# Kernel optimization log

Hardware: AMD Instinct MI355X
Metric: run time of the kernel (lower is better)

The kernel has to match this reference:

```python
import jax, jax.numpy as jnp
import numpy as np

B, T, C = 2, 2048, 1024
H, D = 16, 64
EPS = 1e-05
SCALE = 1.0 / np.sqrt(D)


def _rmsnorm(x, w):
    # normalize over last dim (head_dim)
    return w * (x * jax.lax.rsqrt(jnp.mean(x * x, axis=-1, keepdims=True) + EPS))


def setup_inputs() -> dict:
    key = jax.random.key(0)
    ks = jax.random.split(key, 8)
    x = jax.random.normal(ks[0], (B, T, C), dtype=jnp.float32)
    # causal mask, 1 = attend, 0 = masked
    attention_mask = jnp.tril(jnp.ones((T, T), dtype=jnp.int32))[None, None]
    s = 1.0 / np.sqrt(C)
    Wq = jax.random.normal(ks[1], (C, H * D), dtype=jnp.float32) * s
    Wk = jax.random.normal(ks[2], (C, H * D), dtype=jnp.float32) * s
    Wv = jax.random.normal(ks[3], (C, H * D), dtype=jnp.float32) * s
    Wo = jax.random.normal(ks[4], (H * D, C), dtype=jnp.float32) * s
    q_norm_w = jnp.ones((D,), dtype=jnp.float32)
    k_norm_w = jnp.ones((D,), dtype=jnp.float32)
    gate = jnp.ones((1, H, 1, 1), dtype=jnp.float32)
    return {"x": x, "attention_mask": attention_mask, "Wq": Wq, "Wk": Wk,
            "Wv": Wv, "Wo": Wo, "q_norm_w": q_norm_w, "k_norm_w": k_norm_w,
            "gate": gate}


def reference(x, attention_mask, Wq, Wk, Wv, Wo, q_norm_w, k_norm_w, gate):
    Bx, Tx, Cx = x.shape
    vx = x @ Wv                                   # [B,T,H*D] (kept for value residual)
    q = (x @ Wq).reshape(Bx, Tx, H, D).transpose(0, 2, 1, 3)  # [B,H,T,D]
    k = (x @ Wk).reshape(Bx, Tx, H, D).transpose(0, 2, 1, 3)
    v = vx.reshape(Bx, Tx, H, D).transpose(0, 2, 1, 3)
    q = _rmsnorm(q, q_norm_w)
    k = _rmsnorm(k, k_norm_w)
    att = jnp.einsum('bhqd,bhkd->bhqk', q, k) * SCALE
    att = jnp.where(attention_mask == 0, -jnp.inf, att)
    att = jax.nn.softmax(att, axis=-1)
    att = att * gate                              # per-head gating after softmax
    out = jnp.einsum('bhqk,bhkd->bhqd', att, v)
    out = out.transpose(0, 2, 1, 3).reshape(Bx, Tx, Cx)
    out = out + vx                                # value residual
    out = out @ Wo
    return out
```

## Files before the change

kernel.cpp:

```cpp
#include <hip/hip_runtime.h>

#define T_SEQ 2048
#define CDIM 1024
#define NHEAD 16
#define HDIM 64
#define BATCH 2
#define EPSV 1e-5f
#define SCALE 0.125f
#define LOG2E 1.44269504088896f
#define SMAX 16.0f

typedef __attribute__((ext_vector_type(8))) short bf16x8;
typedef __attribute__((ext_vector_type(4))) float f32x4;

__device__ __forceinline__ float b2f(short s) {
  unsigned u = ((unsigned)(unsigned short)s) << 16;
  return __builtin_bit_cast(float, u);
}
__device__ __forceinline__ short f2b(float f) {
  unsigned u = __builtin_bit_cast(unsigned, f);
  unsigned r = (u + 0x7fffu + ((u >> 16) & 1u)) >> 16;
  return (short)r;
}
__device__ __forceinline__ unsigned cvt_pk_bf16(float a, float b) {
  unsigned r;
  asm("v_cvt_pk_bf16_f32 %0, %1, %2" : "=v"(r) : "v"(a), "v"(b));
  return r;
}

__device__ __forceinline__ void gld16(const void* g, void* l) {
  __builtin_amdgcn_global_load_lds((const __attribute__((address_space(1))) unsigned*)g,
                                   (__attribute__((address_space(3))) unsigned*)l, 16, 0, 0);
}

__device__ __forceinline__ int gswz(int row) { return ((row >> 1) ^ (row >> 3)) & 3; }

__device__ __forceinline__ void stage_sw(short* lds, const char* gbase, int gstride,
                                         int w, int l) {
#pragma unroll
  for (int i = 0; i < 2; ++i) {
    int chunk = w * 2048 + i * 1024 + l * 16;
    int row = chunk >> 7;
    int bir = chunk & 127;
    const char* src = gbase + (size_t)row * gstride + (bir ^ ((row & 7) << 4));
    gld16(src, (char*)lds + chunk);
  }
}
__device__ __forceinline__ void stage_sw8(short* lds, const char* gbase, int gstride,
                                          int w, int l) {
  int chunk = w * 1024 + l * 16;
  int row = chunk >> 7;
  int bir = chunk & 127;
  const char* src = gbase + (size_t)row * gstride + (bir ^ ((row & 7) << 4));
  gld16(src, (char*)lds + chunk);
}

__global__ __launch_bounds__(256) void prep(const float* __restrict__ x,
                                            const float* __restrict__ Wq,
                                            const float* __restrict__ Wk,
                                            const float* __restrict__ Wv,
                                            const float* __restrict__ Wo,
                                            short* __restrict__ xb,
                                            short* __restrict__ WT) {
  __shared__ float tile[64][65];
  const int bid = blockIdx.x;
  if (bid < 2048) {
    size_t i = ((size_t)bid * 256 + threadIdx.x) * 8;
    float4 a = *(const float4*)&x[i];
    float4 b = *(const float4*)&x[i + 4];
    short4 lo, hi;
    lo.x = f2b(a.x); lo.y = f2b(a.y); lo.z = f2b(a.z); lo.w = f2b(a.w);
    hi.x = f2b(b.x); hi.y = f2b(b.y); hi.z = f2b(b.z); hi.w = f2b(b.w);
    *(short4*)&xb[i] = lo;
    *(short4*)&xb[i + 4] = hi;
    return;
  }
  const int t = bid - 2048;
  const int z = t >> 8, rem = t & 255;
  const float* W = (z == 0) ? Wq : (z == 1) ? Wk : (z == 2) ? Wv : Wo;
  const int r0 = (rem >> 4) * 64, c0 = (rem & 15) * 64;
  const int tr = threadIdx.x >> 4, tc4 = (threadIdx.x & 15) * 4;
#pragma unroll
  for (int i = 0; i < 4; ++i) {
    float4 v = *(const float4*)&W[(size_t)(r0 + tr + i * 16) * 1024 + c0 + tc4];
    tile[tr + i * 16][tc4 + 0] = v.x;
    tile[tr + i * 16][tc4 + 1] = v.y;
    tile[tr + i * 16][tc4 + 2] = v.z;
    tile[tr + i * 16][tc4 + 3] = v.w;
  }
  __syncthreads();
#pragma unroll
  for (int i = 0; i < 4; ++i) {
    int n = tr + i * 16;
    short4 o;
    o.x = f2b(tile[tc4 + 0][n]);
    o.y = f2b(tile[tc4 + 1][n]);
    o.z = f2b(tile[tc4 + 2][n]);
    o.w = f2b(tile[tc4 + 3][n]);
    *(short4*)&WT[((size_t)(z * 1024) + c0 + n) * 1024 + r0 + tc4] = o;
  }
}

template <int BN, bool F32OUT, bool NORM>
__global__ __launch_bounds__(256) void gemm_bf16(const short* __restrict__ A,
                                                 const short* __restrict__ Bt,
                                                 void* __restrict__ Cv,
                                                 const float* __restrict__ qw,
                                                 const float* __restrict__ kw,
                                                 int M, int N, int K, int nbx) {
  constexpr int NFR = BN / 32;
  constexpr int BITERS = BN / 64;
  __shared__ __attribute__((aligned(16))) short As[3][4096];
  __shared__ __attribute__((aligned(16))) short Bs[3][BN * 32];
  const int tid = threadIdx.x;
  const int w = tid >> 6, l = tid & 63;
  const int g = l >> 4, c = l & 15;
  const int wm = w >> 1, wn = w & 1;
  const int xcd = blockIdx.x & 7;
  const int i = blockIdx.x >> 3;
  const int bx = i >> 2;
  const int by = xcd * 4 + (i & 3);
  const int m0 = by * 128, n0 = bx * BN;
  const char* Ab = (const char*)A;
  const char* Bb = (const char*)Bt;

  auto stage = [&](int k0, int buf) {
#pragma unroll
    for (int ii = 0; ii < 2; ++ii) {
      int ci = w * 128 + ii * 64 + l;
      int row = ci >> 2, c4 = ci & 3;
      gld16(Ab + ((size_t)(m0 + row) * K + k0) * 2 + ((c4 ^ gswz(row)) << 4),
            (char*)As[buf] + (w * 2048 + ii * 1024));
    }
#pragma unroll
    for (int ii = 0; ii < BITERS; ++ii) {
      int ci = w * (64 * BITERS) + ii * 64 + l;
      int row = ci >> 2, c4 = ci & 3;
      gld16(Bb + ((size_t)(n0 + row) * K + k0) * 2 + ((c4 ^ gswz(row)) << 4),
            (char*)Bs[buf] + (w * (1024 * BITERS) + ii * 1024));
    }
  };

  f32x4 acc[4][NFR];
#pragma unroll
  for (int mt = 0; mt < 4; ++mt)
#pragma unroll
    for (int nt = 0; nt < NFR; ++nt) {
      f32x4 z = {0.f, 0.f, 0.f, 0.f};
      acc[mt][nt] = z;
    }

  const int NT = K >> 5;
  stage(0, 0);
  stage(32, 1);
  if constexpr (BITERS == 2) asm volatile("s_waitcnt vmcnt(4)" ::: "memory");
  else                       asm volatile("s_waitcnt vmcnt(3)" ::: "memory");
  __builtin_amdgcn_s_barrier();
  __builtin_amdgcn_sched_barrier(0);

  int cbuf = 0;
  for (int t = 0; t < NT; ++t) {
    int tgt = cbuf + 2; if (tgt >= 3) tgt -= 3;
    if (t + 2 < NT) stage((t + 2) << 5, tgt);
    bf16x8 a[4], bf[NFR];
#pragma unroll
    for (int mt = 0; mt < 4; ++mt) {
      const int row = wm * 64 + mt * 16 + c;
      a[mt] = *(const bf16x8*)&As[cbuf][row * 32 + ((g ^ gswz(row)) << 3)];
    }
#pragma unroll
    for (int nt = 0; nt < NFR; ++nt) {
      const int row = wn * (BN / 2) + nt * 16 + c;
      bf[nt] = *(const bf16x8*)&Bs[cbuf][row * 32 + ((g ^ gswz(row)) << 3)];
    }
    __builtin_amdgcn_s_setprio(1);
#pragma unroll
    for (int mt = 0; mt < 4; ++mt)
#pragma unroll
      for (int nt = 0; nt < NFR; ++nt)
        acc[mt][nt] = __builtin_amdgcn_mfma_f32_16x16x32_bf16(a[mt], bf[nt], acc[mt][nt], 0, 0, 0);
    __builtin_amdgcn_s_setprio(0);
    if (t + 1 < NT) {
      if (t + 2 < NT) {
        if constexpr (BITERS == 2) asm volatile("s_waitcnt vmcnt(4)" ::: "memory");
        else                       asm volatile("s_waitcnt vmcnt(3)" ::: "memory");
      } else {
        asm volatile("s_waitcnt vmcnt(0)" ::: "memory");
      }
      __builtin_amdgcn_s_barrier();
      __builtin_amdgcn_sched_barrier(0);
    }
    cbuf = cbuf + 1; if (cbuf >= 3) cbuf -= 3;
  }

  if constexpr (NORM) {
    if (n0 < 2048) {
      const float* wgt = (n0 < 1024) ? qw : kw;
      const float scl = (n0 < 1024) ? SCALE * LOG2E : 1.f;
      float w4[NFR];
#pragma unroll
      for (int nt = 0; nt < NFR; ++nt) w4[nt] = wgt[nt * 16 + c] * scl;
#pragma unroll
      for (int mt = 0; mt < 4; ++mt)
#pragma unroll
        for (int r = 0; r < 4; ++r) {
          float s = 0.f;
#pragma unroll
          for (int nt = 0; nt < NFR; ++nt) s += acc[mt][nt][r] * acc[mt][nt][r];
          s += __shfl_xor(s, 1);
          s += __shfl_xor(s, 2);
          s += __shfl_xor(s, 4);
          s += __shfl_xor(s, 8);
          const float rstd = rsqrtf(s * (1.0f / 64.0f) + EPSV);
#pragma unroll
          for (int nt = 0; nt < NFR; ++nt) acc[mt][nt][r] *= rstd * w4[nt];
        }
    }
  }

  if constexpr (F32OUT) {
    float* C = (float*)Cv;
#pragma unroll
    for (int mt = 0; mt < 4; ++mt)
#pragma unroll
      for (int nt = 0; nt < NFR; ++nt)
#pragma unroll
        for (int r = 0; r < 4; ++r)
          C[(size_t)(m0 + wm * 64 + mt * 16 + 4 * g + r) * N + n0 + wn * (BN / 2) + nt * 16 + c] =
              acc[mt][nt][r];
  } else {
    short* C = (short*)Cv;
#pragma unroll
    for (int mt = 0; mt < 4; ++mt)
#pragma unroll
      for (int nt = 0; nt < NFR; ++nt)
#pragma unroll
        for (int r = 0; r < 4; ++r)
          C[(size_t)(m0 + wm * 64 + mt * 16 + 4 * g + r) * N + n0 + wn * (BN / 2) + nt * 16 + c] =
              f2b(acc[mt][nt][r]);
  }
}

__global__ __launch_bounds__(256) void vt_kernel(const short* __restrict__ QKV,
                                                 short* __restrict__ VT) {
  __shared__ short tile[64][66];
  const int t0 = blockIdx.x * 64;
  const int h = blockIdx.y, b = blockIdx.z;
  const int tid = threadIdx.x;
  const int r = tid >> 3, c8 = (tid & 7) * 8;
#pragma unroll
  for (int p = 0; p < 2; ++p) {
    int row = r + p * 32;
    bf16x8 v = *(const bf16x8*)&QKV[(size_t)(b * T_SEQ + t0 + row) * 3072 + 2048 + h * 64 + c8];
#pragma unroll
    for (int j = 0; j < 8; ++j) tile[row][c8 + j] = v[j];
  }
  __syncthreads();
#pragma unroll
  for (int p = 0; p < 2; ++p) {
    int d = r + p * 32;
    short o[8];
#pragma unroll
    for (int j = 0; j < 8; ++j) o[j] = tile[c8 + j][d];
    *(bf16x8*)&VT[((size_t)(b * NHEAD + h) * 64 + d) * T_SEQ + t0 + c8] = *(bf16x8*)o;
  }
}

__global__ __launch_bounds__(512, 4) void attn_fwd(const short* __restrict__ QKV,
                                                   const short* __restrict__ VT,
                                                   const float* __restrict__ gate,
                                                   short* __restrict__ Ob) {
  __shared__ __attribute__((aligned(16))) short pool[40960];

  const int bid = blockIdx.x;
  const int xcd = bid & 7, s = bid >> 3;
  const int t8 = (s >> 2) & 7;
  const int Q16 = (s < 32) ? 15 - t8 : t8;
  const int bh = xcd * 4 + (s & 3);
  const int h = bh & 15, b = bh >> 4;
  const int q0 = Q16 * 128;
  const int nkt = 2 * Q16 + 2;
  const int tid = threadIdx.x;
  const int w = tid >> 6, l = tid & 63;
  const int g = l >> 4, c = l & 15;

  const char* qkb = (const char*)QKV;
  const char* kbase = qkb + ((size_t)(b * T_SEQ) * 3072 + 1024 + h * 64) * 2;
  const char* vtb = (const char*)VT + ((size_t)(b * NHEAD + h) * 64) * T_SEQ * 2;
  const float gh = gate[h];

  stage_sw(pool, qkb + ((size_t)(b * T_SEQ + q0) * 3072 + h * 64) * 2, 3072 * 2, w, l);
  stage_sw8(pool + 8192, kbase, 3072 * 2, w, l);
  stage_sw8(pool + 24576, vtb, T_SEQ * 2, w, l);
  stage_sw8(pool + 8192 + 4096, kbase + (size_t)64 * 3072 * 2, 3072 * 2, w, l);
  stage_sw8(pool + 24576 + 4096, vtb + (size_t)64 * 2, T_SEQ * 2, w, l);
  asm volatile("s_waitcnt vmcnt(4)" ::: "memory");
  __builtin_amdgcn_sched_barrier(0);

  bf16x8 qf[2];
  {
    const int row = w * 16 + c;
#pragma unroll
    for (int ks = 0; ks < 2; ++ks)
      qf[ks] = *(const bf16x8*)&pool[row * 64 + ((ks * 32 + g * 8) ^ ((row & 7) << 3))];
  }

  const char* poolb = (const char*)pool;
  const int bc = (c >> 2) & 1;
  const int swz_g = (g ^ (c & 3)) << 4;
  const int kvoff[2] = {c * 128 + swz_g + (bc << 6),
                        c * 128 + swz_g + ((1 ^ bc) << 6)};
  const int pboff[2] = {w * 2048 + kvoff[0], w * 2048 + kvoff[1]};
  const int cc = (c >> 1) & 3;
  const int pinv = w * 2048 + c * 128 + ((g & 1) << 3) + ((((g >> 1) ^ c) & 1) << 4);
  int p_off[4];
#pragma unroll
  for (int mt = 0; mt < 4; ++mt) p_off[mt] = pinv + ((mt ^ cc) << 5);

  bf16x8 onesf;
#pragma unroll
  for (int j = 0; j < 8; ++j) onesf[j] = (short)0x3F80;

  f32x4 oacc[4];
#pragma unroll
  for (int dt = 0; dt < 4; ++dt) {
    f32x4 z = {0.f, 0.f, 0.f, 0.f};
    oacc[dt] = z;
  }
  f32x4 oacc4 = {0.f, 0.f, 0.f, 0.f};

#define ATTN_TILE(BUF_, KT_)                                                              \
  {                                                                                       \
    constexpr int BUF = (BUF_);                                                           \
    const int kt = (KT_);                                                                 \
    const int dq = q0 + w * 16 - kt * 64;                                                 \
    if (dq > -16) {                                                                       \
      f32x4 sacc[4];                                                                      \
      _Pragma("unroll") for (int mt = 0; mt < 4; ++mt) {                                  \
        f32x4 z = {-SMAX, -SMAX, -SMAX, -SMAX};                                           \
        sacc[mt] = z;                                                                     \
      }                                                                                   \
      __builtin_amdgcn_s_setprio(1);                                                      \
      _Pragma("unroll") for (int mt = 0; mt < 4; ++mt) {                                  \
        _Pragma("unroll") for (int ks = 0; ks < 2; ++ks) {                                \
          bf16x8 kf = *(const bf16x8*)(poolb + 16384 + BUF * 8192 + mt * 2048 +           \
                                       kvoff[ks]);                                        \
          sacc[mt] = __builtin_amdgcn_mfma_f32_16x16x32_bf16(kf, qf[ks], sacc[mt],        \
                                                             0, 0, 0);                    \
        }                                                                                 \
      }                                                                                   \
      __builtin_amdgcn_s_setprio(0);                                                      \
      bf16x8 vf[4][2];                                                                    \
      _Pragma("unroll") for (int dt = 0; dt < 4; ++dt)                                    \
        _Pragma("unroll") for (int ks = 0; ks < 2; ++ks)                                  \
          vf[dt][ks] = *(const bf16x8*)(poolb + 49152 + BUF * 8192 + dt * 2048 +          \
                                        kvoff[ks]);                                       \
      if (dq < 63) {                                                                      \
        _Pragma("unroll") for (int mt = 0; mt < 4; ++mt)                                  \
          _Pragma("unroll") for (int r = 0; r < 4; ++r)                                   \
            if (mt * 16 + 4 * g + r > dq + c) sacc[mt][r] = -1e30f;                       \
      }                                                                                   \
      _Pragma("unroll") for (int mt = 0; mt < 4; ++mt) {                                  \
        float p0 = exp2f(sacc[mt][0]);                                                    \
        float p1 = exp2f(sacc[mt][1]);                                                    \
        float p2 = exp2f(sacc[mt][2]);                                                    \
        float p3 = exp2f(sacc[mt][3]);                                                    \
        uint2 pk;                                                                         \
        pk.x = cvt_pk_bf16(p0, p1);                                                       \
        pk.y = cvt_pk_bf16(p2, p3);                                                       \
        *(uint2*)((char*)pool + p_off[mt]) = pk;                                          \
      }                                                                                   \
      bf16x8 pb[2];                                                                       \
      _Pragma("unroll") for (int ks = 0; ks < 2; ++ks)                                    \
        pb[ks] = *(const bf16x8*)(poolb + pboff[ks]);                                     \
      __builtin_amdgcn_s_setprio(1);                                                      \
      _Pragma("unroll") for (int dt = 0; dt < 4; ++dt)                                    \
        _Pragma("unroll") for (int ks = 0; ks < 2; ++ks)                                  \
          oacc[dt] = __builtin_amdgcn_mfma_f32_16x16x32_bf16(vf[dt][ks], pb[ks],          \
                                                             oacc[dt], 0, 0, 0);          \
      oacc4 = __builtin_amdgcn_mfma_f32_16x16x32_bf16(onesf, pb[0], oacc4, 0, 0, 0);      \
      oacc4 = __builtin_amdgcn_mfma_f32_16x16x32_bf16(onesf, pb[1], oacc4, 0, 0, 0);      \
      __builtin_amdgcn_s_setprio(0);                                                      \
    }                                                                                     \
  }

#define ATTN_PAIR(B_, T0_)                                                                \
  {                                                                                       \
    constexpr int PB = (B_);                                                              \
    const int pt0 = (T0_);                                                                \
    asm volatile("s_waitcnt vmcnt(0)" ::: "memory");                                      \
    __builtin_amdgcn_s_barrier();                                                         \
    __builtin_amdgcn_sched_barrier(0);                                                    \
    if (pt0 + 2 < nkt) {                                                                  \
      constexpr int TB = PB ^ 2;                                                          \
      stage_sw8(pool + 8192 + TB * 4096, kbase + (size_t)(pt0 + 2) * 64 * 3072 * 2,       \
                3072 * 2, w, l);                                                          \
      stage_sw8(pool + 24576 + TB * 4096, vtb + (size_t)(pt0 + 2) * 64 * 2,               \
                T_SEQ * 2, w, l);                                                         \
      stage_sw8(pool + 8192 + (TB + 1) * 4096, kbase + (size_t)(pt0 + 3) * 64 * 3072 * 2, \
                3072 * 2, w, l);                                                          \
      stage_sw8(pool + 24576 + (TB + 1) * 4096, vtb + (size_t)(pt0 + 3) * 64 * 2,         \
                T_SEQ * 2, w, l);                                                         \
    }                                                                                     \
    ATTN_TILE(PB, pt0);                                                                   \
    ATTN_TILE(PB + 1, pt0 + 1);                                                           \
  }

  int t0 = 0;
  for (; t0 + 4 <= nkt; t0 += 4) {
    ATTN_PAIR(0, t0);
    ATTN_PAIR(2, t0 + 2);
  }
  if (t0 < nkt) ATTN_PAIR(0, t0);
#undef ATTN_PAIR
#undef ATTN_TILE

  const float gl = gh / oacc4[0];
  const int qrow = q0 + w * 16 + c;
  const short* Vr = QKV + (size_t)(b * T_SEQ + qrow) * 3072 + 2048 + h * 64;
  short* Oro = Ob + (size_t)(b * T_SEQ + qrow) * 1024 + h * 64;
#pragma unroll
  for (int dt = 0; dt < 4; ++dt) {
    const int d0 = dt * 16 + 4 * g;
    short4 vres = *(const short4*)&Vr[d0];
    short4 o;
    o.x = f2b(oacc[dt][0] * gl + b2f(vres.x));
    o.y = f2b(oacc[dt][1] * gl + b2f(vres.y));
    o.z = f2b(oacc[dt][2] * gl + b2f(vres.z));
    o.w = f2b(oacc[dt][3] * gl + b2f(vres.w));
    *(short4*)&Oro[d0] = o;
  }
}

extern "C" void kernel_launch(void* const* d_in, const int* in_sizes, int n_in,
                              void* d_out, int out_size, void* d_ws, size_t ws_size,
                              hipStream_t stream) {
  const float* x  = (const float*)d_in[0];
  const float* Wq = (const float*)d_in[2];
  const float* Wk = (const float*)d_in[3];
  const float* Wv = (const float*)d_in[4];
  const float* Wo = (const float*)d_in[5];
  const float* qw = (const float*)d_in[6];
  const float* kw = (const float*)d_in[7];
  const float* gate = (const float*)d_in[8];
  float* out = (float*)d_out;

  char* ws = (char*)d_ws;
  short* xb  = (short*)ws;
  short* WT  = (short*)(ws + ((size_t)8 << 20));
  short* QKV = (short*)(ws + ((size_t)16 << 20));
  short* VTb = (short*)(ws + ((size_t)40 << 20));
  short* Obf = (short*)(ws + ((size_t)48 << 20));

  const int M = BATCH * T_SEQ;

  prep<<<3072, 256, 0, stream>>>(x, Wq, Wk, Wv, Wo, xb, WT);
  gemm_bf16<128, false, true><<<768, 256, 0, stream>>>(xb, WT, QKV, qw, kw, M, 3072, CDIM, 24);
  vt_kernel<<<dim3(32, 16, 2), 256, 0, stream>>>(QKV, VTb);
  attn_fwd<<<512, 512, 0, stream>>>(QKV, VTb, gate, Obf);
  gemm_bf16<64, true, false><<<512, 256, 0, stream>>>(Obf, WT + (size_t)3072 * 1024, out,
                                                      nullptr, nullptr, M, CDIM, CDIM, 16);
}
```

Baseline: 109.7 us.

## Process two 16-row query subtiles per wave, halving attention block threads

Attention block shrinks from 8 waves to 4 waves, each handling 32 query rows as two 16-row subtiles. Every K and V fragment read from LDS now feeds two MFMAs, which roughly halves LDS fragment traffic per FLOP. Staging loops are widened so 256 threads load the same tiles. In exchange each wave holds twice the accumulators and registers, and occupancy drops (launch bounds 256,2), so there are fewer waves to hide latency. Causal skip granularity also coarsens to 32 rows.

New measurement: 117.9 us. 1.07x slower.

```diff
diff --git a/kernel.cpp b/kernel.cpp
--- a/kernel.cpp
+++ b/kernel.cpp
@@ -46,13 +46,16 @@
     gld16(src, (char*)lds + chunk);
   }
 }
-__device__ __forceinline__ void stage_sw8(short* lds, const char* gbase, int gstride,
-                                          int w, int l) {
-  int chunk = w * 1024 + l * 16;
-  int row = chunk >> 7;
-  int bir = chunk & 127;
-  const char* src = gbase + (size_t)row * gstride + (bir ^ ((row & 7) << 4));
-  gld16(src, (char*)lds + chunk);
+__device__ __forceinline__ void stage_q(short* lds, const char* gbase, int gstride,
+                                        int w, int l) {
+#pragma unroll
+  for (int i = 0; i < 4; ++i) {
+    int chunk = w * 4096 + i * 1024 + l * 16;
+    int row = chunk >> 7;
+    int bir = chunk & 127;
+    const char* src = gbase + (size_t)row * gstride + (bir ^ ((row & 7) << 4));
+    gld16(src, (char*)lds + chunk);
+  }
 }
 
 __global__ __launch_bounds__(256) void prep(const float* __restrict__ x,
@@ -266,7 +269,7 @@
   }
 }
 
-__global__ __launch_bounds__(512, 4) void attn_fwd(const short* __restrict__ QKV,
+__global__ __launch_bounds__(256, 2) void attn_fwd(const short* __restrict__ QKV,
                                                    const short* __restrict__ VT,
                                                    const float* __restrict__ gate,
                                                    short* __restrict__ Ob) {
@@ -289,20 +292,21 @@
   const char* vtb = (const char*)VT + ((size_t)(b * NHEAD + h) * 64) * T_SEQ * 2;
   const float gh = gate[h];
 
-  stage_sw(pool, qkb + ((size_t)(b * T_SEQ + q0) * 3072 + h * 64) * 2, 3072 * 2, w, l);
-  stage_sw8(pool + 8192, kbase, 3072 * 2, w, l);
-  stage_sw8(pool + 24576, vtb, T_SEQ * 2, w, l);
-  stage_sw8(pool + 8192 + 4096, kbase + (size_t)64 * 3072 * 2, 3072 * 2, w, l);
-  stage_sw8(pool + 24576 + 4096, vtb + (size_t)64 * 2, T_SEQ * 2, w, l);
-  asm volatile("s_waitcnt vmcnt(4)" ::: "memory");
+  stage_q(pool, qkb + ((size_t)(b * T_SEQ + q0) * 3072 + h * 64) * 2, 3072 * 2, w, l);
+  stage_sw(pool + 8192, kbase, 3072 * 2, w, l);
+  stage_sw(pool + 24576, vtb, T_SEQ * 2, w, l);
+  stage_sw(pool + 8192 + 4096, kbase + (size_t)64 * 3072 * 2, 3072 * 2, w, l);
+  stage_sw(pool + 24576 + 4096, vtb + (size_t)64 * 2, T_SEQ * 2, w, l);
+  asm volatile("s_waitcnt vmcnt(8)" ::: "memory");
   __builtin_amdgcn_sched_barrier(0);
 
-  bf16x8 qf[2];
-  {
-    const int row = w * 16 + c;
+  bf16x8 qf[2][2];
+#pragma unroll
+  for (int st = 0; st < 2; ++st) {
+    const int row = w * 32 + st * 16 + c;
 #pragma unroll
     for (int ks = 0; ks < 2; ++ks)
-      qf[ks] = *(const bf16x8*)&pool[row * 64 + ((ks * 32 + g * 8) ^ ((row & 7) << 3))];
+      qf[st][ks] = *(const bf16x8*)&pool[row * 64 + ((ks * 32 + g * 8) ^ ((row & 7) << 3))];
   }
 
   const char* poolb = (const char*)pool;
@@ -310,43 +314,57 @@
   const int swz_g = (g ^ (c & 3)) << 4;
   const int kvoff[2] = {c * 128 + swz_g + (bc << 6),
                         c * 128 + swz_g + ((1 ^ bc) << 6)};
-  const int pboff[2] = {w * 2048 + kvoff[0], w * 2048 + kvoff[1]};
+  int pboff[2][2], p_off[2][4];
   const int cc = (c >> 1) & 3;
-  const int pinv = w * 2048 + c * 128 + ((g & 1) << 3) + ((((g >> 1) ^ c) & 1) << 4);
-  int p_off[4];
-#pragma unroll
-  for (int mt = 0; mt < 4; ++mt) p_off[mt] = pinv + ((mt ^ cc) << 5);
+  const int pinv0 = c * 128 + ((g & 1) << 3) + ((((g >> 1) ^ c) & 1) << 4);
+#pragma unroll
+  for (int st = 0; st < 2; ++st) {
+    const int sbase = w * 4096 + st * 2048;
+#pragma unroll
+    for (int ks = 0; ks < 2; ++ks) pboff[st][ks] = sbase + kvoff[ks];
+#pragma unroll
+    for (int mt = 0; mt < 4; ++mt) p_off[st][mt] = sbase + pinv0 + ((mt ^ cc) << 5);
+  }
 
   bf16x8 onesf;
 #pragma unroll
   for (int j = 0; j < 8; ++j) onesf[j] = (short)0x3F80;
 
-  f32x4 oacc[4];
-#pragma unroll
-  for (int dt = 0; dt < 4; ++dt) {
+  f32x4 oacc[2][4];
+#pragma unroll
+  for (int st = 0; st < 2; ++st)
+#pragma unroll
+    for (int dt = 0; dt < 4; ++dt) {
+      f32x4 z = {0.f, 0.f, 0.f, 0.f};
+      oacc[st][dt] = z;
+    }
+  f32x4 oacc4[2];
+#pragma unroll
+  for (int st = 0; st < 2; ++st) {
     f32x4 z = {0.f, 0.f, 0.f, 0.f};
-    oacc[dt] = z;
-  }
-  f32x4 oacc4 = {0.f, 0.f, 0.f, 0.f};
+    oacc4[st] = z;
+  }
 
 #define ATTN_TILE(BUF_, KT_)                                                              \
   {                                                                                       \
     constexpr int BUF = (BUF_);                                                           \
     const int kt = (KT_);                                                                 \
-    const int dq = q0 + w * 16 - kt * 64;                                                 \
-    if (dq > -16) {                                                                       \
-      f32x4 sacc[4];                                                                      \
-      _Pragma("unroll") for (int mt = 0; mt < 4; ++mt) {                                  \
-        f32x4 z = {-SMAX, -SMAX, -SMAX, -SMAX};                                           \
-        sacc[mt] = z;                                                                     \
-      }                                                                                   \
+    const int dqw = q0 + w * 32 - kt * 64;        \
+    if (dqw + 16 > -16) {                                                                 \
+      f32x4 sacc[2][4];                                                                   \
+      _Pragma("unroll") for (int st = 0; st < 2; ++st)                                    \
+        _Pragma("unroll") for (int mt = 0; mt < 4; ++mt) {                                \
+          f32x4 z = {-SMAX, -SMAX, -SMAX, -SMAX};                                         \
+          sacc[st][mt] = z;                                                               \
+        }                                                                                 \
       __builtin_amdgcn_s_setprio(1);                                                      \
       _Pragma("unroll") for (int mt = 0; mt < 4; ++mt) {                                  \
         _Pragma("unroll") for (int ks = 0; ks < 2; ++ks) {                                \
           bf16x8 kf = *(const bf16x8*)(poolb + 16384 + BUF * 8192 + mt * 2048 +           \
                                        kvoff[ks]);                                        \
-          sacc[mt] = __builtin_amdgcn_mfma_f32_16x16x32_bf16(kf, qf[ks], sacc[mt],        \
-                                                             0, 0, 0);                    \
+          _Pragma("unroll") for (int st = 0; st < 2; ++st)                                \
+            sacc[st][mt] = __builtin_amdgcn_mfma_f32_16x16x32_bf16(kf, qf[st][ks],        \
+                                                                   sacc[st][mt], 0, 0, 0);\
         }                                                                                 \
       }                                                                                   \
       __builtin_amdgcn_s_setprio(0);                                                      \
@@ -355,31 +373,41 @@
         _Pragma("unroll") for (int ks = 0; ks < 2; ++ks)                                  \
           vf[dt][ks] = *(const bf16x8*)(poolb + 49152 + BUF * 8192 + dt * 2048 +          \
                                         kvoff[ks]);                                       \
-      if (dq < 63) {                                                                      \
-        _Pragma("unroll") for (int mt = 0; mt < 4; ++mt)                                  \
-          _Pragma("unroll") for (int r = 0; r < 4; ++r)                                   \
-            if (mt * 16 + 4 * g + r > dq + c) sacc[mt][r] = -1e30f;                       \
+      _Pragma("unroll") for (int st = 0; st < 2; ++st) {                                  \
+        const int dqs = dqw + st * 16;                                                    \
+        if (dqs < 63) {                                                                   \
+          _Pragma("unroll") for (int mt = 0; mt < 4; ++mt)                                \
+            _Pragma("unroll") for (int r = 0; r < 4; ++r)                                 \
+              if (mt * 16 + 4 * g + r > dqs + c) sacc[st][mt][r] = -1e30f;                \
+        }                                                                                 \
+        _Pragma("unroll") for (int mt = 0; mt < 4; ++mt) {                                \
+          float p0 = exp2f(sacc[st][mt][0]);                                              \
+          float p1 = exp2f(sacc[st][mt][1]);                                              \
+          float p2 = exp2f(sacc[st][mt][2]);                                              \
+          float p3 = exp2f(sacc[st][mt][3]);                                              \
+          uint2 pk;                                                                       \
+          pk.x = cvt_pk_bf16(p0, p1);                                                     \
+          pk.y = cvt_pk_bf16(p2, p3);                                                     \
+          *(uint2*)((char*)pool + p_off[st][mt]) = pk;                                    \
+        }                                                                                 \
       }                                                                                   \
-      _Pragma("unroll") for (int mt = 0; mt < 4; ++mt) {                                  \
-        float p0 = exp2f(sacc[mt][0]);                                                    \
-        float p1 = exp2f(sacc[mt][1]);                                                    \
-        float p2 = exp2f(sacc[mt][2]);                                                    \
-        float p3 = exp2f(sacc[mt][3]);                                                    \
-        uint2 pk;                                                                         \
-        pk.x = cvt_pk_bf16(p0, p1);                                                       \
-        pk.y = cvt_pk_bf16(p2, p3);                                                       \
-        *(uint2*)((char*)pool + p_off[mt]) = pk;                                          \
-      }                                                                                   \
-      bf16x8 pb[2];                                                                       \
-      _Pragma("unroll") for (int ks = 0; ks < 2; ++ks)                                    \
-        pb[ks] = *(const bf16x8*)(poolb + pboff[ks]);                                     \
+      bf16x8 pb[2][2];                                                                    \
+      _Pragma("unroll") for (int st = 0; st < 2; ++st)                                    \
+        _Pragma("unroll") for (int ks = 0; ks < 2; ++ks)                                  \
+          pb[st][ks] = *(const bf16x8*)(poolb + pboff[st][ks]);                           \
       __builtin_amdgcn_s_setprio(1);                                                      \
       _Pragma("unroll") for (int dt = 0; dt < 4; ++dt)                                    \
         _Pragma("unroll") for (int ks = 0; ks < 2; ++ks)                                  \
-          oacc[dt] = __builtin_amdgcn_mfma_f32_16x16x32_bf16(vf[dt][ks], pb[ks],          \
-                                                             oacc[dt], 0, 0, 0);          \
-      oacc4 = __builtin_amdgcn_mfma_f32_16x16x32_bf16(onesf, pb[0], oacc4, 0, 0, 0);      \
-      oacc4 = __builtin_amdgcn_mfma_f32_16x16x32_bf16(onesf, pb[1], oacc4, 0, 0, 0);      \
+          _Pragma("unroll") for (int st = 0; st < 2; ++st)                                \
+            oacc[st][dt] = __builtin_amdgcn_mfma_f32_16x16x32_bf16(vf[dt][ks],            \
+                                                                   pb[st][ks],           \
+                                                                   oacc[st][dt], 0, 0, 0);\
+      _Pragma("unroll") for (int st = 0; st < 2; ++st) {                                  \
+        oacc4[st] = __builtin_amdgcn_mfma_f32_16x16x32_bf16(onesf, pb[st][0],             \
+                                                            oacc4[st], 0, 0, 0);          \
+        oacc4[st] = __builtin_amdgcn_mfma_f32_16x16x32_bf16(onesf, pb[st][1],             \
+                                                            oacc4[st], 0, 0, 0);          \
+      }                                                                                   \
       __builtin_amdgcn_s_setprio(0);                                                      \
     }                                                                                     \
   }
@@ -393,14 +421,14 @@
     __builtin_amdgcn_sched_barrier(0);                                                    \
     if (pt0 + 2 < nkt) {                                                                  \
       constexpr int TB = PB ^ 2;                                                          \
-      stage_sw8(pool + 8192 + TB * 4096, kbase + (size_t)(pt0 + 2) * 64 * 3072 * 2,       \
-                3072 * 2, w, l);                                                          \
-      stage_sw8(pool + 24576 + TB * 4096, vtb + (size_t)(pt0 + 2) * 64 * 2,               \
-                T_SEQ * 2, w, l);                                                         \
-      stage_sw8(pool + 8192 + (TB + 1) * 4096, kbase + (size_t)(pt0 + 3) * 64 * 3072 * 2, \
-                3072 * 2, w, l);                                                          \
-      stage_sw8(pool + 24576 + (TB + 1) * 4096, vtb + (size_t)(pt0 + 3) * 64 * 2,         \
-                T_SEQ * 2, w, l);                                                         \
+      stage_sw(pool + 8192 + TB * 4096, kbase + (size_t)(pt0 + 2) * 64 * 3072 * 2,        \
+               3072 * 2, w, l);                                                           \
+      stage_sw(pool + 24576 + TB * 4096, vtb + (size_t)(pt0 + 2) * 64 * 2,                \
+               T_SEQ * 2, w, l);                                                          \
+      stage_sw(pool + 8192 + (TB + 1) * 4096, kbase + (size_t)(pt0 + 3) * 64 * 3072 * 2,  \
+               3072 * 2, w, l);                                                           \
+      stage_sw(pool + 24576 + (TB + 1) * 4096, vtb + (size_t)(pt0 + 3) * 64 * 2,          \
+               T_SEQ * 2, w, l);                                                          \
     }                                                                                     \
     ATTN_TILE(PB, pt0);                                                                   \
     ATTN_TILE(PB + 1, pt0 + 1);                                                           \
@@ -415,20 +443,23 @@
 #undef ATTN_PAIR
 #undef ATTN_TILE
 
-  const float gl = gh / oacc4[0];
-  const int qrow = q0 + w * 16 + c;
-  const short* Vr = QKV + (size_t)(b * T_SEQ + qrow) * 3072 + 2048 + h * 64;
-  short* Oro = Ob + (size_t)(b * T_SEQ + qrow) * 1024 + h * 64;
-#pragma unroll
-  for (int dt = 0; dt < 4; ++dt) {
-    const int d0 = dt * 16 + 4 * g;
-    short4 vres = *(const short4*)&Vr[d0];
-    short4 o;
-    o.x = f2b(oacc[dt][0] * gl + b2f(vres.x));
-    o.y = f2b(oacc[dt][1] * gl + b2f(vres.y));
-    o.z = f2b(oacc[dt][2] * gl + b2f(vres.z));
-    o.w = f2b(oacc[dt][3] * gl + b2f(vres.w));
-    *(short4*)&Oro[d0] = o;
+#pragma unroll
+  for (int st = 0; st < 2; ++st) {
+    const float gl = gh / oacc4[st][0];
+    const int qrow = q0 + w * 32 + st * 16 + c;
+    const short* Vr = QKV + (size_t)(b * T_SEQ + qrow) * 3072 + 2048 + h * 64;
+    short* Oro = Ob + (size_t)(b * T_SEQ + qrow) * 1024 + h * 64;
+#pragma unroll
+    for (int dt = 0; dt < 4; ++dt) {
+      const int d0 = dt * 16 + 4 * g;
+      short4 vres = *(const short4*)&Vr[d0];
+      short4 o;
+      o.x = f2b(oacc[st][dt][0] * gl + b2f(vres.x));
+      o.y = f2b(oacc[st][dt][1] * gl + b2f(vres.y));
+      o.z = f2b(oacc[st][dt][2] * gl + b2f(vres.z));
+      o.w = f2b(oacc[st][dt][3] * gl + b2f(vres.w));
+      *(short4*)&Oro[d0] = o;
+    }
   }
 }
 
@@ -457,7 +488,7 @@
   prep<<<3072, 256, 0, stream>>>(x, Wq, Wk, Wv, Wo, xb, WT);
   gemm_bf16<128, false, true><<<768, 256, 0, stream>>>(xb, WT, QKV, qw, kw, M, 3072, CDIM, 24);
   vt_kernel<<<dim3(32, 16, 2), 256, 0, stream>>>(QKV, VTb);
-  attn_fwd<<<512, 512, 0, stream>>>(QKV, VTb, gate, Obf);
+  attn_fwd<<<512, 256, 0, stream>>>(QKV, VTb, gate, Obf);
   gemm_bf16<64, true, false><<<512, 256, 0, stream>>>(Obf, WT + (size_t)3072 * 1024, out,
                                                       nullptr, nullptr, M, CDIM, CDIM, 16);
 }
```
